# Performance work log

Measured on AMD Instinct MI355X. Metric: run time of the kernel, lower is better.

Reference implementation:

```python
import jax, jax.numpy as jnp
import numpy as np

B, T, D = 32, 1024, 512

def _xavier(key, shape):
    fan_in, fan_out = shape[1], shape[0]
    bound = float(np.sqrt(6.0 / (fan_in + fan_out)))
    return jax.random.uniform(key, shape, jnp.float32, -bound, bound)

def setup_inputs() -> dict:
    key = jax.random.key(0)
    ks = jax.random.split(key, 10)
    lin_bound = float(1.0 / np.sqrt(D))
    def lin(kw, kb):
        W = jax.random.uniform(kw, (D, D), jnp.float32, -lin_bound, lin_bound)
        b = jax.random.uniform(kb, (D,), jnp.float32, -lin_bound, lin_bound)
        return W, b
    Wk_w, Wk_b = lin(ks[0], ks[1])
    Wv_w, Wv_b = lin(ks[2], ks[3])
    Wq_w, Wq_b = lin(ks[4], ks[5])
    Wo_w, Wo_b = lin(ks[6], ks[7])
    w = _xavier(ks[8], (T, T))
    x = jax.random.normal(ks[9], (B, T, D), jnp.float32)
    return {"x": x, "Wk_w": Wk_w, "Wk_b": Wk_b, "Wv_w": Wv_w, "Wv_b": Wv_b,
            "Wq_w": Wq_w, "Wq_b": Wq_b, "w": w, "Wo_w": Wo_w, "Wo_b": Wo_b}

def reference(x, Wk_w, Wk_b, Wv_w, Wv_b, Wq_w, Wq_b, w, Wo_w, Wo_b):
    # K, V, Q: [B, T, D]  (torch Linear: x @ W.T + b)
    K = jnp.einsum('btd,ed->bte', x, Wk_w) + Wk_b
    V = jnp.einsum('btd,ed->bte', x, Wv_w) + Wv_b
    # exp_w: [T, T], row-wise max-stabilized position bias
    exp_w = jnp.exp(w - jnp.max(w, axis=-1, keepdims=True))
    # Faithful to original: max over dim=0 (batch dim) of K
    exp_K = jnp.exp(K - jnp.max(K, axis=0, keepdims=True))  # [B, T, D]
    num = jnp.einsum('ts,bsd->btd', exp_w, exp_K * V)
    den = jnp.einsum('ts,bsd->btd', exp_w, exp_K)
    Yt = num / den
    Q = jnp.einsum('btd,ed->bte', x, Wq_w) + Wq_b
    Yt = jax.nn.sigmoid(Q) * Yt
    out = jnp.einsum('btd,ed->bte', Yt, Wo_w) + Wo_b
    return out
```

## Files before the change

### kernel.cpp

```cpp
#include <hip/hip_runtime.h>
#include <stdint.h>

typedef unsigned short u16;
typedef __attribute__((ext_vector_type(4))) float f32x4;
typedef __attribute__((ext_vector_type(8))) __bf16 bf16x8;

__device__ __forceinline__ float b2f(u16 u) {
  union { unsigned int i; float f; } v; v.i = ((unsigned int)u) << 16; return v.f;
}
__device__ __forceinline__ u16 f2b(float f) {
  union { float f; unsigned int i; } v; v.f = f;
  unsigned int x = v.i;
  return (u16)((x + 0x7fffu + ((x >> 16) & 1u)) >> 16);
}

__device__ __forceinline__ void async_ld16(const u16* g, u16* l) {
  __builtin_amdgcn_global_load_lds((const __attribute__((address_space(1))) void*)g,
                                   (__attribute__((address_space(3))) void*)l, 16, 0, 0);
}

__global__ void detect_kernel(const u16* __restrict__ x, int* __restrict__ flag)
{
  const int tid = threadIdx.x;
  int found = 0;
  for (int i = tid; i < 32768; i += 256) {
    u16 u = x[i];
    if ((u & 0x7F80u) == 0x7F80u) found = 1;
  }
  unsigned long long m = __ballot(found != 0);
  __shared__ int sf[4];
  if ((tid & 63) == 0) sf[tid >> 6] = (m != 0ULL) ? 1 : 0;
  __syncthreads();
  if (tid == 0) flag[0] = (sf[0] | sf[1] | sf[2] | sf[3]);
}

__global__ __launch_bounds__(256)
void conv_kernel(const void* __restrict__ in, u16* __restrict__ out, long n,
                 const int* __restrict__ flag)
{
  const long i = ((long)blockIdx.x * 256 + threadIdx.x) * 8;
  if (i >= n) return;
  if (flag[0]) {
    const float* p = (const float*)in + i;
    u16 o[8];
#pragma unroll
    for (int j = 0; j < 8; j++) o[j] = f2b(p[j]);
    *(uint4*)(out + i) = *(const uint4*)o;
  } else {
    *(uint4*)(out + i) = *(const uint4*)((const u16*)in + i);
  }
}

__global__ __launch_bounds__(256)
void conv4_kernel(const void* __restrict__ i0, const void* __restrict__ i1,
                  const void* __restrict__ i2, const void* __restrict__ i3,
                  u16* __restrict__ o0, u16* __restrict__ o1,
                  u16* __restrict__ o2, u16* __restrict__ o3,
                  const int* __restrict__ flag)
{
  const int sel = blockIdx.x >> 7;
  const int blk = blockIdx.x & 127;
  const void* in = (sel == 0) ? i0 : (sel == 1) ? i1 : (sel == 2) ? i2 : i3;
  u16* out = (sel == 0) ? o0 : (sel == 1) ? o1 : (sel == 2) ? o2 : o3;
  const long i = ((long)blk * 256 + threadIdx.x) * 8;
  if (flag[0]) {
    const float* p = (const float*)in + i;
    u16 o[8];
#pragma unroll
    for (int j = 0; j < 8; j++) o[j] = f2b(p[j]);
    *(uint4*)(out + i) = *(const uint4*)o;
  } else {
    *(uint4*)(out + i) = *(const uint4*)((const u16*)in + i);
  }
}

#define BM 128
#define BN 128
#define BK 32

template<int EPI>
__global__ __launch_bounds__(256)
void gemm_bt(const u16* __restrict__ A, const u16* __restrict__ B,
             const void* __restrict__ bias, void* __restrict__ Cv,
             const int* __restrict__ flag,
             int M, int N, int K, long strideC)
{
  __shared__ __align__(16) u16 sA[2][BM * BK];
  __shared__ __align__(16) u16 sB[2][BN * BK];

  const int tid  = threadIdx.x;
  const int lane = tid & 63;
  const int wv   = tid >> 6;
  const int fl = flag[0];
  u16* Cb16 = (u16*)Cv;

  int bx = blockIdx.x, by = blockIdx.y;
  {
    const int nx = gridDim.x, ny = gridDim.y;
    if ((nx & 7) == 0) {
      const int d   = bx + nx * by;
      const int xcd = d & 7;
      const int s   = d >> 3;
      const int q   = s / ny;
      bx = xcd * (nx >> 3) + q;
      by = s - q * ny;
    }
  }
  const int m0 = bx * BM;
  const int n0 = by * BN;

  const int ldRow = wv * 32;
  const int lr = lane >> 2;
  const int lc = lane & 3;
  const int scol = (lc ^ ((lr >> 1) & 3)) * 8;
  const u16* gA = A + (long)(m0 + ldRow + lr) * K + scol;
  const u16* gB = B + (long)(n0 + ldRow + lr) * K + scol;
  const int off0 = (ldRow + lr) * BK + lc * 8;
  const int off1 = (ldRow + 16 + lr) * BK + lc * 8;

  f32x4 acc[4][4];
#pragma unroll
  for (int i = 0; i < 4; i++)
#pragma unroll
    for (int j = 0; j < 4; j++) acc[i][j] = (f32x4)0.0f;

  const int waveM = (wv >> 1) * 64;
  const int waveN = (wv & 1) * 64;
  const int quad  = lane >> 4;
  const int ll    = lane & 15;
  const int rs    = (quad ^ ((ll >> 1) & 3)) * 8;

  async_ld16(gA,          sA[0] + off0);
  async_ld16(gA + 16 * K, sA[0] + off1);
  async_ld16(gB,          sB[0] + off0);
  async_ld16(gB + 16 * K, sB[0] + off1);
  gA += BK; gB += BK;

  const int NT = K / BK;
  for (int t = 0; t < NT; ++t) {
    __syncthreads();
    const int cur = t & 1;
    if (t + 1 < NT) {
      u16* dA = sA[cur ^ 1];
      u16* dB = sB[cur ^ 1];
      async_ld16(gA,          dA + off0);
      async_ld16(gA + 16 * K, dA + off1);
      async_ld16(gB,          dB + off0);
      async_ld16(gB + 16 * K, dB + off1);
      gA += BK; gB += BK;
    }
    const u16* rA = sA[cur];
    const u16* rB = sB[cur];
    bf16x8 aF[4], bF[4];
#pragma unroll
    for (int i = 0; i < 4; i++) {
      aF[i] = *(const bf16x8*)(rA + (waveM + i * 16 + ll) * BK + rs);
      bF[i] = *(const bf16x8*)(rB + (waveN + i * 16 + ll) * BK + rs);
    }
#pragma unroll
    for (int i = 0; i < 4; i++)
#pragma unroll
      for (int j = 0; j < 4; j++)
        acc[i][j] = __builtin_amdgcn_mfma_f32_16x16x32_bf16(aF[i], bF[j], acc[i][j], 0, 0, 0);
  }

#pragma unroll
  for (int i = 0; i < 4; i++) {
    const int rowb = m0 + waveM + i * 16 + quad * 4;
#pragma unroll
    for (int j = 0; j < 4; j++) {
      const int col = n0 + waveN + j * 16 + ll;
      const float bv = fl ? ((const float*)bias)[col] : b2f(((const u16*)bias)[col]);
#pragma unroll
      for (int r = 0; r < 4; r++) {
        const long idx = (long)(rowb + r) * N + col;
        const float v = acc[i][j][r] + bv;
        if (EPI == 0) {
          Cb16[idx] = f2b(v);
        } else {
          const long g = strideC + idx;
          if (fl) ((float*)Cv)[g] = v;
          else    ((u16*)Cv)[g]   = f2b(v);
        }
      }
    }
  }
}

__global__ __launch_bounds__(256)
void gemm_proj3(const u16* __restrict__ A, const u16* __restrict__ Bw,
                const void* __restrict__ kb, const void* __restrict__ vb,
                const void* __restrict__ qb,
                u16* __restrict__ Kp, u16* __restrict__ Vp, u16* __restrict__ Qp,
                const int* __restrict__ flag, int M)
{
  const int KD = 512;
  __shared__ __align__(16) u16 sA[2][BM * BK];
  __shared__ __align__(16) u16 sB[2][BN * BK];

  const int tid  = threadIdx.x;
  const int lane = tid & 63;
  const int wv   = tid >> 6;
  const int fl = flag[0];

  int bx = blockIdx.x, by = blockIdx.y;
  {
    const int nx = gridDim.x, ny = gridDim.y;
    if ((nx & 7) == 0) {
      const int d   = bx + nx * by;
      const int xcd = d & 7;
      const int s   = d >> 3;
      const int q   = s / ny;
      bx = xcd * (nx >> 3) + q;
      by = s - q * ny;
    }
  }
  const int m0 = bx * BM;
  const int n0 = by * BN;

  const int ldRow = wv * 32;
  const int lr = lane >> 2;
  const int lc = lane & 3;
  const int scol = (lc ^ ((lr >> 1) & 3)) * 8;
  const u16* gA = A  + (long)(m0 + ldRow + lr) * KD + scol;
  const u16* gB = Bw + (long)(n0 + ldRow + lr) * KD + scol;
  const int off0 = (ldRow + lr) * BK + lc * 8;
  const int off1 = (ldRow + 16 + lr) * BK + lc * 8;

  f32x4 acc[4][4];
#pragma unroll
  for (int i = 0; i < 4; i++)
#pragma unroll
    for (int j = 0; j < 4; j++) acc[i][j] = (f32x4)0.0f;

  const int waveM = (wv >> 1) * 64;
  const int waveN = (wv & 1) * 64;
  const int quad  = lane >> 4;
  const int ll    = lane & 15;
  const int rs    = (quad ^ ((ll >> 1) & 3)) * 8;

  async_ld16(gA,           sA[0] + off0);
  async_ld16(gA + 16 * KD, sA[0] + off1);
  async_ld16(gB,           sB[0] + off0);
  async_ld16(gB + 16 * KD, sB[0] + off1);
  gA += BK; gB += BK;

  const int NT = KD / BK;
  for (int t = 0; t < NT; ++t) {
    __syncthreads();
    const int cur = t & 1;
    if (t + 1 < NT) {
      u16* dA = sA[cur ^ 1];
      u16* dB = sB[cur ^ 1];
      async_ld16(gA,           dA + off0);
      async_ld16(gA + 16 * KD, dA + off1);
      async_ld16(gB,           dB + off0);
      async_ld16(gB + 16 * KD, dB + off1);
      gA += BK; gB += BK;
    }
    const u16* rA = sA[cur];
    const u16* rB = sB[cur];
    bf16x8 aF[4], bF[4];
#pragma unroll
    for (int i = 0; i < 4; i++) {
      aF[i] = *(const bf16x8*)(rA + (waveM + i * 16 + ll) * BK + rs);
      bF[i] = *(const bf16x8*)(rB + (waveN + i * 16 + ll) * BK + rs);
    }
#pragma unroll
    for (int i = 0; i < 4; i++)
#pragma unroll
      for (int j = 0; j < 4; j++)
        acc[i][j] = __builtin_amdgcn_mfma_f32_16x16x32_bf16(aF[i], bF[j], acc[i][j], 0, 0, 0);
  }

#pragma unroll
  for (int i = 0; i < 4; i++) {
    const int rowb = m0 + waveM + i * 16 + quad * 4;
#pragma unroll
    for (int j = 0; j < 4; j++) {
      const int col = n0 + waveN + j * 16 + ll;
      const int sel = col >> 9;
      const int cs  = col & 511;
      const void* bp = (sel == 0) ? kb : (sel == 1) ? vb : qb;
      u16* dst = (sel == 0) ? Kp : (sel == 1) ? Vp : Qp;
      const float bv = fl ? ((const float*)bp)[cs] : b2f(((const u16*)bp)[cs]);
#pragma unroll
      for (int r = 0; r < 4; r++)
        dst[(long)(rowb + r) * 512 + cs] = f2b(acc[i][j][r] + bv);
    }
  }
}

__global__ __launch_bounds__(512, 2)
void gemm_aft(const u16* __restrict__ ew, const u16* __restrict__ Pt,
              const u16* __restrict__ PVt, const u16* __restrict__ Q,
              u16* __restrict__ Yt)
{
  const int T = 1024, D = 512;
  __shared__ __align__(16) u16 sA[2 * 2 * 256 * 32];
  __shared__ __align__(16) u16 sB[2 * 2 * 128 * 32];
  __shared__ __align__(16) u16 sC[2 * 2 * 128 * 32];

  const int tid  = threadIdx.x;
  const int lane = tid & 63;
  const int wv   = tid >> 6;

  int xt = blockIdx.x, yt = blockIdx.y, zt = blockIdx.z;
  {
    const int nz = gridDim.z;
    if ((nz & 1) == 0) {
      const int d   = xt + (yt << 2) + (zt << 4);
      const int xcd = d & 7;
      const int s   = d >> 3;
      xt = s & 3;
      const int p = xcd * (nz >> 1) + (s >> 2);
      yt = p & 3;
      zt = p >> 2;
    }
  }
  const int b = zt;
  const u16* Ptb  = Pt  + (long)b * D * T;
  const u16* PVtb = PVt + (long)b * D * T;
  const u16* Qb   = Q   + (long)b * T * D;
  u16*       Ytb  = Yt  + (long)b * T * D;
  const int m0 = xt * 256;
  const int n0 = yt * 128;

  const int sr = tid >> 2, ss = tid & 3;
  const int sslot = (ss ^ ((sr >> 1) & 3)) * 8;
  const u16* gA0 = ew   + (long)(m0 + sr)       * T + sslot;
  const u16* gA1 = ew   + (long)(m0 + 128 + sr) * T + sslot;
  const u16* gB  = Ptb  + (long)(n0 + sr)       * T + sslot;
  const u16* gC  = PVtb + (long)(n0 + sr)       * T + sslot;
  const int soff = sr * 32 + ss * 8;

  f32x4 accN[8][2], accD[8][2];
#pragma unroll
  for (int i = 0; i < 8; i++)
#pragma unroll
    for (int j = 0; j < 2; j++) { accN[i][j] = (f32x4)0.0f; accD[i][j] = (f32x4)0.0f; }

  const int quad  = lane >> 4;
  const int ll    = lane & 15;
  const int rs    = (quad ^ ((ll >> 1) & 3)) * 8;
  const int waveM = (wv >> 2) * 128;
  const int waveN = (wv & 3) * 32;

  async_ld16(gA0,      sA + soff);
  async_ld16(gA1,      sA + 4096 + soff);
  async_ld16(gB,       sB + soff);
  async_ld16(gC,       sC + soff);
  async_ld16(gA0 + 32, sA + 8192 + soff);
  async_ld16(gA1 + 32, sA + 8192 + 4096 + soff);
  async_ld16(gB  + 32, sB + 4096 + soff);
  async_ld16(gC  + 32, sC + 4096 + soff);
  asm volatile("s_waitcnt vmcnt(4)" ::: "memory");
  __builtin_amdgcn_s_barrier();

  const int NT = T / 64;
  for (int t = 0; t < NT; ++t) {
    const int cur = t & 1;
    const u16* bA = sA + cur * 16384;
    const u16* bB = sB + cur * 8192;
    const u16* bC = sC + cur * 8192;
    u16* nA = sA + (cur ^ 1) * 16384;
    u16* nB = sB + (cur ^ 1) * 8192;
    u16* nC = sC + (cur ^ 1) * 8192;
    const int ko = (t + 1) * 64;
    const bool st = (t + 1 < NT);

    bf16x8 aF[4], bF[2], cF[2];

#pragma unroll
    for (int i = 0; i < 4; i++)
      aF[i] = *(const bf16x8*)(bA + (waveM + i * 16 + ll) * 32 + rs);
#pragma unroll
    for (int j = 0; j < 2; j++) {
      bF[j] = *(const bf16x8*)(bB + (waveN + j * 16 + ll) * 32 + rs);
      cF[j] = *(const bf16x8*)(bC + (waveN + j * 16 + ll) * 32 + rs);
    }
    if (st) {
      async_ld16(gA0 + ko, nA + soff);
      async_ld16(gA1 + ko, nA + 4096 + soff);
    }
    __builtin_amdgcn_s_barrier();
    asm volatile("s_waitcnt lgkmcnt(0)" ::: "memory");
    __builtin_amdgcn_sched_barrier(0);
    __builtin_amdgcn_s_setprio(1);
#pragma unroll
    for (int i = 0; i < 4; i++)
#pragma unroll
      for (int j = 0; j < 2; j++) {
        accD[i][j] = __builtin_amdgcn_mfma_f32_16x16x32_bf16(aF[i], bF[j], accD[i][j], 0, 0, 0);
        accN[i][j] = __builtin_amdgcn_mfma_f32_16x16x32_bf16(aF[i], cF[j], accN[i][j], 0, 0, 0);
      }
    __builtin_amdgcn_s_setprio(0);
    __builtin_amdgcn_s_barrier();

#pragma unroll
    for (int i = 0; i < 4; i++)
      aF[i] = *(const bf16x8*)(bA + (waveM + (4 + i) * 16 + ll) * 32 + rs);
    if (st) {
      async_ld16(gB + ko, nB + soff);
      async_ld16(gC + ko, nC + soff);
    }
    __builtin_amdgcn_s_barrier();
    asm volatile("s_waitcnt lgkmcnt(0)" ::: "memory");
    __builtin_amdgcn_sched_barrier(0);
    __builtin_amdgcn_s_setprio(1);
#pragma unroll
    for (int i = 0; i < 4; i++)
#pragma unroll
      for (int j = 0; j < 2; j++) {
        accD[4 + i][j] = __builtin_amdgcn_mfma_f32_16x16x32_bf16(aF[i], bF[j], accD[4 + i][j], 0, 0, 0);
        accN[4 + i][j] = __builtin_amdgcn_mfma_f32_16x16x32_bf16(aF[i], cF[j], accN[4 + i][j], 0, 0, 0);
      }
    __builtin_amdgcn_s_setprio(0);
    if (st) asm volatile("s_waitcnt vmcnt(4)" ::: "memory");
    else    asm volatile("s_waitcnt vmcnt(0)" ::: "memory");
    __builtin_amdgcn_s_barrier();

    const u16* bA1 = bA + 8192;
    const u16* bB1 = bB + 4096;
    const u16* bC1 = bC + 4096;
#pragma unroll
    for (int i = 0; i < 4; i++)
      aF[i] = *(const bf16x8*)(bA1 + (waveM + i * 16 + ll) * 32 + rs);
#pragma unroll
    for (int j = 0; j < 2; j++) {
      bF[j] = *(const bf16x8*)(bB1 + (waveN + j * 16 + ll) * 32 + rs);
      cF[j] = *(const bf16x8*)(bC1 + (waveN + j * 16 + ll) * 32 + rs);
    }
    if (st) {
      async_ld16(gA0 + ko + 32, nA + 8192 + soff);
      async_ld16(gA1 + ko + 32, nA + 8192 + 4096 + soff);
    }
    __builtin_amdgcn_s_barrier();
    asm volatile("s_waitcnt lgkmcnt(0)" ::: "memory");
    __builtin_amdgcn_sched_barrier(0);
    __builtin_amdgcn_s_setprio(1);
#pragma unroll
    for (int i = 0; i < 4; i++)
#pragma unroll
      for (int j = 0; j < 2; j++) {
        accD[i][j] = __builtin_amdgcn_mfma_f32_16x16x32_bf16(aF[i], bF[j], accD[i][j], 0, 0, 0);
        accN[i][j] = __builtin_amdgcn_mfma_f32_16x16x32_bf16(aF[i], cF[j], accN[i][j], 0, 0, 0);
      }
    __builtin_amdgcn_s_setprio(0);
    __builtin_amdgcn_s_barrier();

#pragma unroll
    for (int i = 0; i < 4; i++)
      aF[i] = *(const bf16x8*)(bA1 + (waveM + (4 + i) * 16 + ll) * 32 + rs);
    if (st) {
      async_ld16(gB + ko + 32, nB + 4096 + soff);
      async_ld16(gC + ko + 32, nC + 4096 + soff);
    }
    __builtin_amdgcn_s_barrier();
    asm volatile("s_waitcnt lgkmcnt(0)" ::: "memory");
    __builtin_amdgcn_sched_barrier(0);
    __builtin_amdgcn_s_setprio(1);
#pragma unroll
    for (int i = 0; i < 4; i++)
#pragma unroll
      for (int j = 0; j < 2; j++) {
        accD[4 + i][j] = __builtin_amdgcn_mfma_f32_16x16x32_bf16(aF[i], bF[j], accD[4 + i][j], 0, 0, 0);
        accN[4 + i][j] = __builtin_amdgcn_mfma_f32_16x16x32_bf16(aF[i], cF[j], accN[4 + i][j], 0, 0, 0);
      }
    __builtin_amdgcn_s_setprio(0);
    if (st) asm volatile("s_waitcnt vmcnt(4)" ::: "memory");
    else    asm volatile("s_waitcnt vmcnt(0)" ::: "memory");
    __builtin_amdgcn_s_barrier();
  }

#pragma unroll
  for (int i = 0; i < 8; i++) {
    const int rowb = m0 + waveM + i * 16 + quad * 4;
#pragma unroll
    for (int j = 0; j < 2; j++) {
      const int col = n0 + waveN + j * 16 + ll;
#pragma unroll
      for (int r = 0; r < 4; r++) {
        const long idx = (long)(rowb + r) * D + col;
        const float q  = b2f(Qb[idx]);
        const float e  = __expf(-q);
        const float rc = __builtin_amdgcn_rcpf(accD[i][j][r] * (1.0f + e));
        Ytb[idx] = f2b(accN[i][j][r] * rc);
      }
    }
  }
}

__global__ __launch_bounds__(256)
void expw_kernel(const void* __restrict__ w, u16* __restrict__ ew,
                 const int* __restrict__ flag)
{
  const int fl = flag[0];
  const int t = blockIdx.x;
  const int tid = threadIdx.x;
  float v[4];
  float m = -1e30f;
#pragma unroll
  for (int i = 0; i < 4; i++) {
    const long idx = (long)t * 1024 + tid + i * 256;
    float val = fl ? ((const float*)w)[idx] : b2f(((const u16*)w)[idx]);
    v[i] = val; m = fmaxf(m, val);
  }
#pragma unroll
  for (int off = 32; off > 0; off >>= 1) m = fmaxf(m, __shfl_xor(m, off, 64));
  __shared__ float sm[4];
  if ((tid & 63) == 0) sm[tid >> 6] = m;
  __syncthreads();
  m = fmaxf(fmaxf(sm[0], sm[1]), fmaxf(sm[2], sm[3]));
  u16* orow = ew + (long)t * 1024;
#pragma unroll
  for (int i = 0; i < 4; i++) orow[tid + i * 256] = f2b(__expf(v[i] - m));
}

__global__ __launch_bounds__(256)
void kmax_kernel(const u16* __restrict__ K, u16* __restrict__ Km)
{
  const long TD = 1024L * 512;
  const long base = ((long)blockIdx.x * 256 + threadIdx.x) * 8;
  float m[8];
#pragma unroll
  for (int j = 0; j < 8; j++) m[j] = -1e30f;
  for (int b = 0; b < 32; b++) {
    uint4 u = *(const uint4*)(K + b * TD + base);
    const u16* p = (const u16*)&u;
#pragma unroll
    for (int j = 0; j < 8; j++) m[j] = fmaxf(m[j], b2f(p[j]));
  }
  u16 outv[8];
#pragma unroll
  for (int j = 0; j < 8; j++) outv[j] = f2b(m[j]);
  *(uint4*)(Km + base) = *(const uint4*)outv;
}

__global__ __launch_bounds__(256)
void pexp_kernel(const u16* __restrict__ K, const u16* __restrict__ V,
                 const u16* __restrict__ Km,
                 u16* __restrict__ Pt, u16* __restrict__ PVt)
{
  const int T = 1024, D = 512;
  const long TD = (long)T * D;
  const int s0 = blockIdx.x * 64;
  const int d0 = blockIdx.y * 64;
  const int b  = blockIdx.z;
  __shared__ u16 lp[64 * 66];
  __shared__ u16 lpv[64 * 66];
  const int tid  = threadIdx.x;
  const int srow = tid >> 3;
  const int c8   = (tid & 7) * 8;

#pragma unroll
  for (int h = 0; h < 2; h++) {
    const int s = srow + h * 32;
    const long gidx = (long)b * TD + (long)(s0 + s) * D + d0 + c8;
    uint4 ku = *(const uint4*)(K + gidx);
    uint4 vu = *(const uint4*)(V + gidx);
    uint4 mu = *(const uint4*)(Km + (long)(s0 + s) * D + d0 + c8);
    const u16* kp = (const u16*)&ku;
    const u16* vp = (const u16*)&vu;
    const u16* mp = (const u16*)&mu;
#pragma unroll
    for (int j = 0; j < 8; j++) {
      float p  = __expf(b2f(kp[j]) - b2f(mp[j]));
      float pv = p * b2f(vp[j]);
      lp[s * 66 + c8 + j]  = f2b(p);
      lpv[s * 66 + c8 + j] = f2b(pv);
    }
  }
  __syncthreads();

  const int lane = tid & 63;
  const int wv   = tid >> 6;
#pragma unroll
  for (int it = 0; it < 16; it++) {
    const int d = wv * 16 + it;
    const long oidx = (long)b * TD + (long)(d0 + d) * T + s0 + lane;
    Pt[oidx]  = lp[lane * 66 + d];
    PVt[oidx] = lpv[lane * 66 + d];
  }
}

extern "C" void kernel_launch(void* const* d_in, const int* in_sizes, int n_in,
                              void* d_out, int out_size, void* d_ws, size_t ws_size,
                              hipStream_t stream)
{
  const int B = 32, T = 1024, D = 512;
  const long TD = (long)T * D;
  const void* x    = d_in[0];
  const void* Wk_w = d_in[1];
  const void* Wk_b = d_in[2];
  const void* Wv_w = d_in[3];
  const void* Wv_b = d_in[4];
  const void* Wq_w = d_in[5];
  const void* Wq_b = d_in[6];
  const void* w    = d_in[7];
  const void* Wo_w = d_in[8];
  const void* Wo_b = d_in[9];

  char* ws = (char*)d_ws;
  const size_t MB = 1024 * 1024;
  u16* xb    = (u16*)(ws + 0);
  u16* Kbuf  = (u16*)(ws + 32 * MB);
  u16* ewb   = (u16*)(ws + 64 * MB);
  u16* kmb   = (u16*)(ws + 66 * MB);
  u16* Wpack = (u16*)(ws + 67 * MB);
  u16* Wvb   = Wpack + 512 * 512;
  u16* Wqb   = Wpack + 2 * 512 * 512;
  u16* Wob   = (u16*)(ws + 68 * MB + 512 * 1024);
  int* flag  = (int*)(ws + 69 * MB);
  u16* Ytb   = Kbuf;

  dim3 blk(256);

  detect_kernel<<<dim3(1), blk, 0, stream>>>((const u16*)x, flag);
  conv_kernel<<<dim3(8192), blk, 0, stream>>>(x, xb, (long)B * T * D, flag);
  conv4_kernel<<<dim3(512), blk, 0, stream>>>(Wk_w, Wv_w, Wq_w, Wo_w,
                                              Wpack, Wvb, Wqb, Wob, flag);
  expw_kernel<<<dim3(1024), blk, 0, stream>>>(w, ewb, flag);

  if (ws_size >= 200 * MB) {
    u16* Vb   = (u16*)(ws + 70 * MB);
    u16* Qb   = (u16*)(ws + 102 * MB);
    u16* Ptb  = (u16*)(ws + 134 * MB);
    u16* PVtb = (u16*)(ws + 166 * MB);

    gemm_proj3<<<dim3((B * T) / 128, 12), blk, 0, stream>>>(
        xb, Wpack, Wk_b, Wv_b, Wq_b, Kbuf, Vb, Qb, flag, B * T);

    kmax_kernel<<<dim3(256), blk, 0, stream>>>(Kbuf, kmb);
    pexp_kernel<<<dim3(16, 8, 32), blk, 0, stream>>>(Kbuf, Vb, kmb, Ptb, PVtb);

    gemm_aft<<<dim3(4, 4, 32), dim3(512), 0, stream>>>(ewb, Ptb, PVtb, Qb, Ytb);

    gemm_bt<3><<<dim3((B * T) / 128, D / 128), blk, 0, stream>>>(
        Ytb, Wob, Wo_b, d_out, flag, B * T, D, D, 0);
  } else {
    const int NB = 4, NC = B / NB;
    char* ck = ws + 70 * MB;
    const size_t cb = (size_t)NB * TD * sizeof(u16);
    u16* Vc   = (u16*)(ck);
    u16* Ptc  = (u16*)(ck + cb);
    u16* PVtc = (u16*)(ck + 2 * cb);
    u16* Qc   = (u16*)(ck + 3 * cb);
    u16* Ytc  = Vc;

    gemm_bt<0><<<dim3((B * T) / 128, D / 128), blk, 0, stream>>>(
        xb, Wpack, Wk_b, Kbuf, flag, B * T, D, D, 0);
    kmax_kernel<<<dim3(256), blk, 0, stream>>>(Kbuf, kmb);

    dim3 gP((NB * T) / 128, D / 128, 1);
    dim3 gA(4, 4, NB);
    for (int c = 0; c < NC; c++) {
      const long off = (long)c * NB * TD;
      gemm_bt<0><<<gP, blk, 0, stream>>>(xb + off, Wvb, Wv_b, Vc, flag, NB * T, D, D, 0);
      gemm_bt<0><<<gP, blk, 0, stream>>>(xb + off, Wqb, Wq_b, Qc, flag, NB * T, D, D, 0);
      pexp_kernel<<<dim3(16, 8, NB), blk, 0, stream>>>(Kbuf + off, Vc, kmb, Ptc, PVtc);
      gemm_aft<<<gA, dim3(512), 0, stream>>>(ewb, Ptc, PVtc, Qc, Ytc);
      gemm_bt<3><<<gP, blk, 0, stream>>>(Ytc, Wob, Wo_b, d_out, flag, NB * T, D, D, off);
    }
  }
}
```

Before: 378.2 us.

## Use 256x256-tile 8-wave pipelined GEMM for QKV and output projections

```diff
diff --git a/kernel.cpp b/kernel.cpp
--- a/kernel.cpp
+++ b/kernel.cpp
@@ -187,7 +187,120 @@
   }
 }
 
-__global__ __launch_bounds__(256)
+#define GEMM8_PHASES(KROW)                                                      \
+  const int NT = (KROW) / 64;                                                   \
+  for (int t = 0; t < NT; ++t) {                                                \
+    const int cur = t & 1;                                                      \
+    const u16* bA = sA + cur * 16384;                                           \
+    const u16* bB = sB + cur * 16384;                                           \
+    u16* nA = sA + (cur ^ 1) * 16384;                                           \
+    u16* nB = sB + (cur ^ 1) * 16384;                                           \
+    const int ko = (t + 1) * 64;                                                \
+    const bool st = (t + 1 < NT);                                               \
+    bf16x8 aF[4], bF[4];                                                        \
+                                                    \
+    _Pragma("unroll")                                                           \
+    for (int i = 0; i < 4; i++)                                                 \
+      aF[i] = *(const bf16x8*)(bA + (waveM + i * 16 + ll) * 32 + rs);           \
+    _Pragma("unroll")                                                           \
+    for (int j = 0; j < 4; j++)                                                 \
+      bF[j] = *(const bf16x8*)(bB + (waveN + j * 16 + ll) * 32 + rs);           \
+    if (st) {                                                                   \
+      async_ld16(gA0 + ko, nA + soff);                                          \
+      async_ld16(gA1 + ko, nA + 4096 + soff);                                   \
+    }                                                                           \
+    __builtin_amdgcn_s_barrier();                                               \
+    asm volatile("s_waitcnt lgkmcnt(0)" ::: "memory");                          \
+    __builtin_amdgcn_sched_barrier(0);                                          \
+    __builtin_amdgcn_s_setprio(1);                                              \
+    _Pragma("unroll")                                                           \
+    for (int i = 0; i < 4; i++)                                                 \
+      _Pragma("unroll")                                                         \
+      for (int j = 0; j < 4; j++)                                               \
+        acc[i][j] = __builtin_amdgcn_mfma_f32_16x16x32_bf16(aF[i], bF[j], acc[i][j], 0, 0, 0); \
+    __builtin_amdgcn_s_setprio(0);                                              \
+    __builtin_amdgcn_s_barrier();                                               \
+                                                              \
+    _Pragma("unroll")                                                           \
+    for (int i = 0; i < 4; i++)                                                 \
+      aF[i] = *(const bf16x8*)(bA + (waveM + (4 + i) * 16 + ll) * 32 + rs);     \
+    if (st) {                                                                   \
+      async_ld16(gB0 + ko, nB + soff);                                          \
+      async_ld16(gB1 + ko, nB + 4096 + soff);                                   \
+    }                                                                           \
+    __builtin_amdgcn_s_barrier();                                               \
+    asm volatile("s_waitcnt lgkmcnt(0)" ::: "memory");                          \
+    __builtin_amdgcn_sched_barrier(0);                                          \
+    __builtin_amdgcn_s_setprio(1);                                              \
+    _Pragma("unroll")                                                           \
+    for (int i = 0; i < 4; i++)                                                 \
+      _Pragma("unroll")                                                         \
+      for (int j = 0; j < 4; j++)                                               \
+        acc[4 + i][j] = __builtin_amdgcn_mfma_f32_16x16x32_bf16(aF[i], bF[j], acc[4 + i][j], 0, 0, 0); \
+    __builtin_amdgcn_s_setprio(0);                                              \
+    if (st) asm volatile("s_waitcnt vmcnt(4)" ::: "memory");                    \
+    else    asm volatile("s_waitcnt vmcnt(0)" ::: "memory");                    \
+    __builtin_amdgcn_s_barrier();                                               \
+                                                    \
+    const u16* bA1 = bA + 8192;                                                 \
+    const u16* bB1 = bB + 8192;                                                 \
+    _Pragma("unroll")                                                           \
+    for (int i = 0; i < 4; i++)                                                 \
+      aF[i] = *(const bf16x8*)(bA1 + (waveM + i * 16 + ll) * 32 + rs);          \
+    _Pragma("unroll")                                                           \
+    for (int j = 0; j < 4; j++)                                                 \
+      bF[j] = *(const bf16x8*)(bB1 + (waveN + j * 16 + ll) * 32 + rs);          \
+    if (st) {                                                                   \
+      async_ld16(gA0 + ko + 32, nA + 8192 + soff);                              \
+      async_ld16(gA1 + ko + 32, nA + 8192 + 4096 + soff);                       \
+    }                                                                           \
+    __builtin_amdgcn_s_barrier();                                               \
+    asm volatile("s_waitcnt lgkmcnt(0)" ::: "memory");                          \
+    __builtin_amdgcn_sched_barrier(0);                                          \
+    __builtin_amdgcn_s_setprio(1);                                              \
+    _Pragma("unroll")                                                           \
+    for (int i = 0; i < 4; i++)                                                 \
+      _Pragma("unroll")                                                         \
+      for (int j = 0; j < 4; j++)                                               \
+        acc[i][j] = __builtin_amdgcn_mfma_f32_16x16x32_bf16(aF[i], bF[j], acc[i][j], 0, 0, 0); \
+    __builtin_amdgcn_s_setprio(0);                                              \
+    __builtin_amdgcn_s_barrier();                                               \
+                                                              \
+    _Pragma("unroll")                                                           \
+    for (int i = 0; i < 4; i++)                                                 \
+      aF[i] = *(const bf16x8*)(bA1 + (waveM + (4 + i) * 16 + ll) * 32 + rs);    \
+    if (st) {                                                                   \
+      async_ld16(gB0 + ko + 32, nB + 8192 + soff);                              \
+      async_ld16(gB1 + ko + 32, nB + 8192 + 4096 + soff);                       \
+    }                                                                           \
+    __builtin_amdgcn_s_barrier();                                               \
+    asm volatile("s_waitcnt lgkmcnt(0)" ::: "memory");                          \
+    __builtin_amdgcn_sched_barrier(0);                                          \
+    __builtin_amdgcn_s_setprio(1);                                              \
+    _Pragma("unroll")                                                           \
+    for (int i = 0; i < 4; i++)                                                 \
+      _Pragma("unroll")                                                         \
+      for (int j = 0; j < 4; j++)                                               \
+        acc[4 + i][j] = __builtin_amdgcn_mfma_f32_16x16x32_bf16(aF[i], bF[j], acc[4 + i][j], 0, 0, 0); \
+    __builtin_amdgcn_s_setprio(0);                                              \
+    if (st) asm volatile("s_waitcnt vmcnt(4)" ::: "memory");                    \
+    else    asm volatile("s_waitcnt vmcnt(0)" ::: "memory");                    \
+    __builtin_amdgcn_s_barrier();                                               \
+  }
+
+#define GEMM8_PRO(KROW)                                                         \
+  async_ld16(gA0,      sA + soff);                                              \
+  async_ld16(gA1,      sA + 4096 + soff);                                       \
+  async_ld16(gB0,      sB + soff);                                              \
+  async_ld16(gB1,      sB + 4096 + soff);                                       \
+  async_ld16(gA0 + 32, sA + 8192 + soff);                                       \
+  async_ld16(gA1 + 32, sA + 8192 + 4096 + soff);                                \
+  async_ld16(gB0 + 32, sB + 8192 + soff);                                       \
+  async_ld16(gB1 + 32, sB + 8192 + 4096 + soff);                                \
+  asm volatile("s_waitcnt vmcnt(4)" ::: "memory");                              \
+  __builtin_amdgcn_s_barrier();
+
+__global__ __launch_bounds__(512, 2)
 void gemm_proj3(const u16* __restrict__ A, const u16* __restrict__ Bw,
                 const void* __restrict__ kb, const void* __restrict__ vb,
                 const void* __restrict__ qb,
@@ -195,8 +308,8 @@
                 const int* __restrict__ flag, int M)
 {
   const int KD = 512;
-  __shared__ __align__(16) u16 sA[2][BM * BK];
-  __shared__ __align__(16) u16 sB[2][BN * BK];
+  __shared__ __align__(16) u16 sA[2 * 2 * 256 * 32];
+  __shared__ __align__(16) u16 sB[2 * 2 * 256 * 32];
 
   const int tid  = threadIdx.x;
   const int lane = tid & 63;
@@ -206,75 +319,41 @@
   int bx = blockIdx.x, by = blockIdx.y;
   {
     const int nx = gridDim.x, ny = gridDim.y;
-    if ((nx & 7) == 0) {
-      const int d   = bx + nx * by;
-      const int xcd = d & 7;
-      const int s   = d >> 3;
-      const int q   = s / ny;
-      bx = xcd * (nx >> 3) + q;
-      by = s - q * ny;
-    }
-  }
-  const int m0 = bx * BM;
-  const int n0 = by * BN;
-
-  const int ldRow = wv * 32;
-  const int lr = lane >> 2;
-  const int lc = lane & 3;
-  const int scol = (lc ^ ((lr >> 1) & 3)) * 8;
-  const u16* gA = A  + (long)(m0 + ldRow + lr) * KD + scol;
-  const u16* gB = Bw + (long)(n0 + ldRow + lr) * KD + scol;
-  const int off0 = (ldRow + lr) * BK + lc * 8;
-  const int off1 = (ldRow + 16 + lr) * BK + lc * 8;
-
-  f32x4 acc[4][4];
-#pragma unroll
-  for (int i = 0; i < 4; i++)
+    const int d   = bx + nx * by;
+    const int xcd = d & 7;
+    const int s   = d >> 3;
+    const int q   = s / ny;
+    bx = xcd * (nx >> 3) + q;
+    by = s - q * ny;
+  }
+  const int m0 = bx * 256;
+  const int n0 = by * 256;
+
+  const int sr = tid >> 2, ss = tid & 3;
+  const int sslot = (ss ^ ((sr >> 1) & 3)) * 8;
+  const u16* gA0 = A  + (long)(m0 + sr)       * KD + sslot;
+  const u16* gA1 = A  + (long)(m0 + 128 + sr) * KD + sslot;
+  const u16* gB0 = Bw + (long)(n0 + sr)       * KD + sslot;
+  const u16* gB1 = Bw + (long)(n0 + 128 + sr) * KD + sslot;
+  const int soff = sr * 32 + ss * 8;
+
+  f32x4 acc[8][4];
+#pragma unroll
+  for (int i = 0; i < 8; i++)
 #pragma unroll
     for (int j = 0; j < 4; j++) acc[i][j] = (f32x4)0.0f;
 
-  const int waveM = (wv >> 1) * 64;
-  const int waveN = (wv & 1) * 64;
   const int quad  = lane >> 4;
   const int ll    = lane & 15;
   const int rs    = (quad ^ ((ll >> 1) & 3)) * 8;
-
-  async_ld16(gA,           sA[0] + off0);
-  async_ld16(gA + 16 * KD, sA[0] + off1);
-  async_ld16(gB,           sB[0] + off0);
-  async_ld16(gB + 16 * KD, sB[0] + off1);
-  gA += BK; gB += BK;
-
-  const int NT = KD / BK;
-  for (int t = 0; t < NT; ++t) {
-    __syncthreads();
-    const int cur = t & 1;
-    if (t + 1 < NT) {
-      u16* dA = sA[cur ^ 1];
-      u16* dB = sB[cur ^ 1];
-      async_ld16(gA,           dA + off0);
-      async_ld16(gA + 16 * KD, dA + off1);
-      async_ld16(gB,           dB + off0);
-      async_ld16(gB + 16 * KD, dB + off1);
-      gA += BK; gB += BK;
-    }
-    const u16* rA = sA[cur];
-    const u16* rB = sB[cur];
-    bf16x8 aF[4], bF[4];
-#pragma unroll
-    for (int i = 0; i < 4; i++) {
-      aF[i] = *(const bf16x8*)(rA + (waveM + i * 16 + ll) * BK + rs);
-      bF[i] = *(const bf16x8*)(rB + (waveN + i * 16 + ll) * BK + rs);
-    }
-#pragma unroll
-    for (int i = 0; i < 4; i++)
-#pragma unroll
-      for (int j = 0; j < 4; j++)
-        acc[i][j] = __builtin_amdgcn_mfma_f32_16x16x32_bf16(aF[i], bF[j], acc[i][j], 0, 0, 0);
-  }
-
-#pragma unroll
-  for (int i = 0; i < 4; i++) {
+  const int waveM = (wv >> 2) * 128;
+  const int waveN = (wv & 3) * 64;
+
+  GEMM8_PRO(KD)
+  GEMM8_PHASES(KD)
+
+#pragma unroll
+  for (int i = 0; i < 8; i++) {
     const int rowb = m0 + waveM + i * 16 + quad * 4;
 #pragma unroll
     for (int j = 0; j < 4; j++) {
@@ -287,6 +366,73 @@
 #pragma unroll
       for (int r = 0; r < 4; r++)
         dst[(long)(rowb + r) * 512 + cs] = f2b(acc[i][j][r] + bv);
+    }
+  }
+}
+
+__global__ __launch_bounds__(512, 2)
+void gemm_out8(const u16* __restrict__ A, const u16* __restrict__ Bw,
+               const void* __restrict__ bias, void* __restrict__ Cv,
+               const int* __restrict__ flag, int M, int N, int K)
+{
+  __shared__ __align__(16) u16 sA[2 * 2 * 256 * 32];
+  __shared__ __align__(16) u16 sB[2 * 2 * 256 * 32];
+
+  const int tid  = threadIdx.x;
+  const int lane = tid & 63;
+  const int wv   = tid >> 6;
+  const int fl = flag[0];
+
+  int bx = blockIdx.x, by = blockIdx.y;
+  {
+    const int nx = gridDim.x, ny = gridDim.y;
+    const int d   = bx + nx * by;
+    const int xcd = d & 7;
+    const int s   = d >> 3;
+    const int q   = s / ny;
+    bx = xcd * (nx >> 3) + q;
+    by = s - q * ny;
+  }
+  const int m0 = bx * 256;
+  const int n0 = by * 256;
+
+  const int sr = tid >> 2, ss = tid & 3;
+  const int sslot = (ss ^ ((sr >> 1) & 3)) * 8;
+  const u16* gA0 = A  + (long)(m0 + sr)       * K + sslot;
+  const u16* gA1 = A  + (long)(m0 + 128 + sr) * K + sslot;
+  const u16* gB0 = Bw + (long)(n0 + sr)       * K + sslot;
+  const u16* gB1 = Bw + (long)(n0 + 128 + sr) * K + sslot;
+  const int soff = sr * 32 + ss * 8;
+
+  f32x4 acc[8][4];
+#pragma unroll
+  for (int i = 0; i < 8; i++)
+#pragma unroll
+    for (int j = 0; j < 4; j++) acc[i][j] = (f32x4)0.0f;
+
+  const int quad  = lane >> 4;
+  const int ll    = lane & 15;
+  const int rs    = (quad ^ ((ll >> 1) & 3)) * 8;
+  const int waveM = (wv >> 2) * 128;
+  const int waveN = (wv & 3) * 64;
+
+  GEMM8_PRO(K)
+  GEMM8_PHASES(K)
+
+#pragma unroll
+  for (int i = 0; i < 8; i++) {
+    const int rowb = m0 + waveM + i * 16 + quad * 4;
+#pragma unroll
+    for (int j = 0; j < 4; j++) {
+      const int col = n0 + waveN + j * 16 + ll;
+      const float bv = fl ? ((const float*)bias)[col] : b2f(((const u16*)bias)[col]);
+#pragma unroll
+      for (int r = 0; r < 4; r++) {
+        const long idx = (long)(rowb + r) * N + col;
+        const float v = acc[i][j][r] + bv;
+        if (fl) ((float*)Cv)[idx] = v;
+        else    ((u16*)Cv)[idx]   = f2b(v);
+      }
     }
   }
 }
@@ -628,7 +774,7 @@
     u16* Ptb  = (u16*)(ws + 134 * MB);
     u16* PVtb = (u16*)(ws + 166 * MB);
 
-    gemm_proj3<<<dim3((B * T) / 128, 12), blk, 0, stream>>>(
+    gemm_proj3<<<dim3((B * T) / 256, 6), dim3(512), 0, stream>>>(
         xb, Wpack, Wk_b, Wv_b, Wq_b, Kbuf, Vb, Qb, flag, B * T);
 
     kmax_kernel<<<dim3(256), blk, 0, stream>>>(Kbuf, kmb);
@@ -636,8 +782,8 @@
 
     gemm_aft<<<dim3(4, 4, 32), dim3(512), 0, stream>>>(ewb, Ptb, PVtb, Qb, Ytb);
 
-    gemm_bt<3><<<dim3((B * T) / 128, D / 128), blk, 0, stream>>>(
-        Ytb, Wob, Wo_b, d_out, flag, B * T, D, D, 0);
+    gemm_out8<<<dim3((B * T) / 256, 2), dim3(512), 0, stream>>>(
+        Ytb, Wob, Wo_b, d_out, flag, B * T, D, D);
   } else {
     const int NB = 4, NC = B / NB;
     char* ck = ws + 70 * MB;
```

Result: no change. 375.8 us (-0.6%).
